# Performance work log

Measured on AMD Instinct MI355X. Metric: run time of the kernel, lower is better.

The kernel has to match this reference:

```python
import jax, jax.numpy as jnp
import numpy as np

N_TRAIN = 2000
N_ATOMS = 30
DIM_D = N_ATOMS * (N_ATOMS - 1) // 2   # 435 pairwise descriptor entries
DIM_I = 3 * N_ATOMS                    # 90 Cartesian dofs
N_PERMS = 12
SIG = 10.0

_ROWS, _COLS = np.tril_indices(N_ATOMS, -1)
_DR = np.arange(DIM_D)


def d_desc_from_comp(Rd):
    # Rd: [n, DIM_D, 3] compact pair derivatives -> full Jacobian [n, DIM_D, DIM_I]
    # each pair (a,b) contributes +d at atom a's 3 dofs and -d at atom b's.
    n = Rd.shape[0]
    out = jnp.zeros((n, DIM_D, N_ATOMS, 3), Rd.dtype)
    out = out.at[:, _DR, _ROWS, :].set(Rd)
    out = out.at[:, _DR, _COLS, :].set(-Rd)
    return out.reshape(n, DIM_D, DIM_I)


def setup_inputs() -> dict:
    key = jax.random.key(0)
    k1, k2 = jax.random.split(key)
    R_desc = jax.random.normal(k1, (N_TRAIN, DIM_D), jnp.float32)
    R_d_desc = jax.random.normal(k2, (N_TRAIN, DIM_D, 3), jnp.float32)
    # Build a permutation-consistent tril_perms_lin (identity + random atom perms).
    rng = np.random.RandomState(0)
    M = np.zeros((N_ATOMS, N_ATOMS), np.int64)
    M[_ROWS, _COLS] = np.arange(DIM_D)
    M[_COLS, _ROWS] = np.arange(DIM_D)
    tril_perms = np.empty((N_PERMS, DIM_D), np.int64)
    for p in range(N_PERMS):
        perm = np.arange(N_ATOMS) if p == 0 else rng.permutation(N_ATOMS)
        tril_perms[p] = M[perm[_ROWS], perm[_COLS]]
    tpl = (tril_perms + np.arange(N_PERMS)[:, None] * DIM_D).flatten(order='F')
    return {
        'R_desc': R_desc,
        'R_d_desc': R_d_desc,
        'tril_perms_lin': jnp.asarray(tpl),
        'j': 0,
    }


def reference(R_desc, R_d_desc, tril_perms_lin, j):
    q = np.sqrt(5.0) / SIG
    # column point j: expanded Jacobian [DIM_D, DIM_I]
    rj_d = d_desc_from_comp(R_d_desc[j][None])[0]
    # permutation-symmetrized descriptor / Jacobian for point j
    rj_desc_perms = jnp.tile(R_desc[j], N_PERMS)[tril_perms_lin].reshape(DIM_D, N_PERMS).T  # [P,D]
    rj_d_perms = jnp.tile(rj_d.T, (1, N_PERMS))[:, tril_perms_lin].reshape(DIM_I, DIM_D, N_PERMS)  # [3N,D,P]
    x_diffs = q * (R_desc[:, None, :] - rj_desc_perms[None])        # [n,P,D]
    x_dists = jnp.linalg.norm(x_diffs, axis=-1)                      # [n,P]
    exp_xs = jnp.exp(-x_dists) * (q * q / 3.0)                       # [n,P]
    exp_xs_1_x_dists = exp_xs * (1.0 + x_dists)                      # [n,P]
    # Matern-5/2 Hessian block assembly
    inner = jnp.einsum('npd,jdp->npj', x_diffs, rj_d_perms)          # [n,P,3N]
    diff_ab = jnp.einsum('npd,npj->ndj', x_diffs * exp_xs[:, :, None], inner)  # [n,D,3N]
    diff_ab = diff_ab - jnp.einsum('jdp,np->ndj', rj_d_perms, exp_xs_1_x_dists)
    Rd_full = d_desc_from_comp(R_d_desc)                             # [n,D,3N]
    k = jnp.einsum('ndj,ndk->nkj', diff_ab, Rd_full)                 # [n,3N,3N]
    return k.reshape(N_TRAIN * DIM_I, DIM_I)
```

## Files before the change

### kernel.cpp

```cpp
#include <hip/hip_runtime.h>
#include <math.h>

#define NA 30
#define ND 435
#define NI 90
#define NP 12
#define NNB (NA-1)

typedef float v2f __attribute__((ext_vector_type(2)));

struct Pre {
  int   pidx[NP][ND];
  int   pinv[NP][ND];
  int   sigma[NP][NA];
  int   sigma_inv[NP][NA];
  int   rowv[ND];
  int   colv[ND];
  int   nbr[NA][NNB];
  float rjp[NP][ND];
  float rdj[ND][3];
  unsigned int gtab[NNB][NP][NA];
  alignas(16) unsigned int stab[NA][NA][NP];
  unsigned int hmask[NA][NA];
};

__device__ __forceinline__ int pair_index(int x, int y) {
  int hi = max(x, y), lo = min(x, y);
  return hi * (hi - 1) / 2 + lo;
}

__global__ void preA_kernel(const int* __restrict__ tpl, Pre* ws) {
  const int tid = threadIdx.x;
  const int nthr = blockDim.x;

  for (int d = tid; d < ND; d += nthr) {
    int a = (int)floorf((1.0f + sqrtf(1.0f + 8.0f * (float)d)) * 0.5f);
    while (a * (a - 1) / 2 > d) --a;
    while ((a + 1) * a / 2 <= d) ++a;
    ws->rowv[d] = a;
    ws->colv[d] = d - a * (a - 1) / 2;
  }
  for (int a = tid; a < NA; a += nthr) {
    int k = 0;
    for (int u = 0; u < NA; ++u)
      if (u != a) ws->nbr[a][k++] = pair_index(a, u);
  }
  for (int idx = tid; idx < NP * ND; idx += nthr) {
    int d = idx / NP, p = idx % NP;
    ws->pidx[p][d] = tpl[idx] - p * ND;
  }
  __syncthreads();
  for (int idx = tid; idx < NP * ND; idx += nthr) {
    int d = idx / NP, p = idx % NP;
    ws->pinv[p][ws->pidx[p][d]] = d;
  }
  for (int idx = tid; idx < NP * NA; idx += nthr) {
    int p = idx / NA, a = idx % NA;
    int u1 = (a == 0) ? 1 : 0;
    int u2 = (a <= 1) ? 2 : 1;
    int e1 = ws->pidx[p][pair_index(a, u1)];
    int e2 = ws->pidx[p][pair_index(a, u2)];
    int r1 = ws->rowv[e1], c1 = ws->colv[e1];
    int r2 = ws->rowv[e2], c2 = ws->colv[e2];
    int sa = (r1 == r2 || r1 == c2) ? r1 : c1;
    ws->sigma[p][a] = sa;
  }
  __syncthreads();
  for (int idx = tid; idx < NP * NA; idx += nthr) {
    int p = idx / NA, a = idx % NA;
    ws->sigma_inv[p][ws->sigma[p][a]] = a;
  }
  __syncthreads();
  for (int it = tid; it < NA * NA; it += nthr) {
    int a = it / NA, a2 = it % NA;
    unsigned m = 0;
#pragma unroll
    for (int p = 0; p < NP; ++p)
      if (ws->sigma[p][a] == a2) m |= (1u << p);
    ws->hmask[a][a2] = m;
  }
}

__global__ void preB_kernel(const float* __restrict__ R_desc,
                            const float* __restrict__ R_d_desc,
                            const int* __restrict__ jptr,
                            Pre* ws) {
  const int gid = blockIdx.x * blockDim.x + threadIdx.x;
  const int gsz = gridDim.x * blockDim.x;
  const int j = *jptr;

  for (int idx = gid; idx < NP * ND; idx += gsz) {
    int p = idx / ND, d = idx % ND;
    ws->rjp[p][d] = R_desc[(size_t)j * ND + ws->pidx[p][d]];
  }
  for (int idx = gid; idx < ND * 3; idx += gsz)
    ((float*)ws->rdj)[idx] = R_d_desc[(size_t)j * (ND * 3) + idx];

  for (int idx = gid; idx < NNB * NP * NA; idx += gsz) {
    int a = idx % NA;
    int r = idx / NA;
    int p = r % NP, k = r / NP;
    int d  = ws->nbr[a][k];
    int di = ws->pinv[p][d];
    int d2 = ws->pidx[p][d];
    int s1 = (ws->rowv[d] == a) ? 1 : 0;
    int s2 = (ws->rowv[d2] == ws->sigma[p][a]) ? 1 : 0;
    unsigned int u = (unsigned)d | ((unsigned)di << 9) | ((unsigned)d2 << 18);
    if (s1) u |= (1u << 27);
    if (s1 == s2) u |= (1u << 28);
    ws->gtab[k][p][a] = u;
  }
  for (int idx = gid; idx < NA * NA * NP; idx += gsz) {
    int p = idx % NP;
    int r = idx / NP;
    int a2 = r % NA, a = r / NA;
    unsigned int u = 0;
    if (ws->sigma[p][a] != a2) {
      int uu = ws->sigma_inv[p][a2];
      int d1 = pair_index(a, uu);
      int d2 = ws->pidx[p][d1];
      int s1 = (ws->rowv[d1] == a) ? 1 : 0;
      int s2 = (ws->rowv[d2] == a2) ? 1 : 0;
      unsigned code = (s1 == s2) ? 1u : 2u;
      u = (unsigned)d1 | ((unsigned)d2 << 9) | (code << 18);
    }
    ws->stab[a][a2][p] = u;
  }
}

__global__ __launch_bounds__(256) void gdml_kernel(
    const float* __restrict__ R_desc,
    const float* __restrict__ R_d_desc,
    const Pre* __restrict__ ws,
    float* __restrict__ out) {
  const int n = blockIdx.x;
  const int tid = threadIdx.x;

  __shared__ float U[NP * ND];
  __shared__ float Rdn_l[ND][3];
  __shared__ float Rdj_l[ND][3];
  __shared__ float v_s[NP][NI];
  __shared__ float inner_s[NP][NI];
  __shared__ float e_s[NP], e1_s[NP];

  float* xd = U;
  float (*Hh)[NP * 9] = (float(*)[NP * 9])U;

  const float q   = 0.22360679774997896f;
  const float qq3 = 0.016666666666666666f;

  for (int idx = tid; idx < ND * 3; idx += 256) {
    ((float*)Rdn_l)[idx] = R_d_desc[(size_t)n * (ND * 3) + idx];
    ((float*)Rdj_l)[idx] = ((const float*)ws->rdj)[idx];
  }
  for (int d = tid; d < ND; d += 256) {
    float rn = R_desc[(size_t)n * ND + d];
#pragma unroll
    for (int p = 0; p < NP; ++p) xd[p * ND + d] = q * (rn - ws->rjp[p][d]);
  }
  __syncthreads();

  {
    int w = tid >> 6, lane = tid & 63;
#pragma unroll
    for (int pp = 0; pp < 3; ++pp) {
      int p = 3 * w + pp;
      float acc = 0.f;
#pragma unroll
      for (int i = 0; i < 7; ++i) {
        int d = lane + 64 * i;
        if (d < ND) { float x = xd[p * ND + d]; acc += x * x; }
      }
      for (int off = 32; off; off >>= 1) acc += __shfl_xor(acc, off);
      if (lane == 0) {
        float dist = sqrtf(acc);
        float e = expf(-dist) * qq3;
        e_s[p] = e;
        e1_s[p] = e * (1.f + dist);
      }
    }
  }
  __syncthreads();

  auto p2_item = [&](int it, float (&h)[9]) {
    int a = it % NA, p = it / NA;
    const float* xdp = xd + p * ND;
    float v0 = 0.f, v1 = 0.f, v2 = 0.f;
    float i0 = 0.f, i1 = 0.f, i2 = 0.f;
    v2f H0 = {0.f, 0.f}, H1 = {0.f, 0.f}, H2 = {0.f, 0.f};
    float Hc0 = 0.f, Hc1 = 0.f, Hc2 = 0.f;
    for (int k = 0; k < NNB; ++k) {
      unsigned int u = ws->gtab[k][p][a];
      int d  = u & 511;
      int di = (u >> 9) & 511;
      int d2 = (u >> 18) & 511;
      float s  = (u & (1u << 27)) ? 1.f : -1.f;
      float sg = (u & (1u << 28)) ? 1.f : -1.f;
      float xv = s * xdp[d];
      float xi = s * xdp[di];
      float n0 = Rdn_l[d][0], n1 = Rdn_l[d][1], n2 = Rdn_l[d][2];
      float jd0 = Rdj_l[d][0], jd1 = Rdj_l[d][1], jd2 = Rdj_l[d][2];
      float jb0 = Rdj_l[d2][0], jb1 = Rdj_l[d2][1], jb2 = Rdj_l[d2][2];
      v0 += xv * n0; v1 += xv * n1; v2 += xv * n2;
      i0 += xi * jd0; i1 += xi * jd1; i2 += xi * jd2;
      float r0 = sg * n0, r1 = sg * n1, r2 = sg * n2;
      v2f jb01 = {jb0, jb1};
      H0 += (v2f){r0, r0} * jb01; Hc0 += r0 * jb2;
      H1 += (v2f){r1, r1} * jb01; Hc1 += r1 * jb2;
      H2 += (v2f){r2, r2} * jb01; Hc2 += r2 * jb2;
    }
    float e = e_s[p];
    v_s[p][3 * a + 0] = e * v0;
    v_s[p][3 * a + 1] = e * v1;
    v_s[p][3 * a + 2] = e * v2;
    inner_s[p][3 * a + 0] = i0;
    inner_s[p][3 * a + 1] = i1;
    inner_s[p][3 * a + 2] = i2;
    h[0] = H0.x; h[1] = H0.y; h[2] = Hc0;
    h[3] = H1.x; h[4] = H1.y; h[5] = Hc1;
    h[6] = H2.x; h[7] = H2.y; h[8] = Hc2;
  };

  float h1[9], h2[9];
  const int it1 = tid;
  const int it2 = tid + 256;
  const bool has2 = (it2 < NP * NA);
  p2_item(it1, h1);
  if (has2) p2_item(it2, h2);
  __syncthreads();

  {
    int a = it1 % NA, p = it1 / NA;
    float* hb = &Hh[a][p * 9];
#pragma unroll
    for (int r = 0; r < 9; ++r) hb[r] = h1[r];
  }
  if (has2) {
    int a = it2 % NA, p = it2 / NA;
    float* hb = &Hh[a][p * 9];
#pragma unroll
    for (int r = 0; r < 9; ++r) hb[r] = h2[r];
  }
  __syncthreads();

  float e1r[NP];
#pragma unroll
  for (int p = 0; p < NP; ++p) e1r[p] = e1_s[p];

  float* outn = out + (size_t)n * (NI * NI);
  for (int it = tid; it < NA * NA; it += 256) {
    int a = it / NA, a2 = it % NA;
    v2f A0 = {0.f, 0.f}, A1 = {0.f, 0.f}, A2 = {0.f, 0.f};
    float B0 = 0.f, B1 = 0.f, B2 = 0.f;
    const uint4* st4 = (const uint4*)&ws->stab[a][a2][0];
    uint4 ua = st4[0], ub = st4[1], uc = st4[2];
    unsigned stv[12] = {ua.x, ua.y, ua.z, ua.w, ub.x, ub.y, ub.z, ub.w,
                        uc.x, uc.y, uc.z, uc.w};
#pragma unroll
    for (int p = 0; p < NP; ++p) {
      float v0 = v_s[p][3 * a + 0];
      float v1 = v_s[p][3 * a + 1];
      float v2v = v_s[p][3 * a + 2];
      float w0 = inner_s[p][3 * a2 + 0];
      float w1 = inner_s[p][3 * a2 + 1];
      float w2 = inner_s[p][3 * a2 + 2];
      v2f w01 = {w0, w1};
      A0 += (v2f){v0, v0} * w01;   B0 += v0 * w2;
      A1 += (v2f){v1, v1} * w01;   B1 += v1 * w2;
      A2 += (v2f){v2v, v2v} * w01; B2 += v2v * w2;
      unsigned u = stv[p];
      unsigned code = (u >> 18) & 3u;
      float e1 = e1r[p];
      float f = (code == 1u) ? -e1 : ((code == 2u) ? e1 : 0.f);
      int d1 = u & 511;
      int d2 = (u >> 9) & 511;
      float r0 = f * Rdn_l[d1][0];
      float r1 = f * Rdn_l[d1][1];
      float r2 = f * Rdn_l[d1][2];
      float j0 = Rdj_l[d2][0], j1 = Rdj_l[d2][1], j2 = Rdj_l[d2][2];
      v2f j01 = {j0, j1};
      A0 += (v2f){r0, r0} * j01;   B0 += r0 * j2;
      A1 += (v2f){r1, r1} * j01;   B1 += r1 * j2;
      A2 += (v2f){r2, r2} * j01;   B2 += r2 * j2;
    }
    unsigned m = ws->hmask[a][a2];
    while (m) {
      int p = __ffs(m) - 1;
      m &= m - 1;
      float e1 = e1r[p];
      const float* hb = &Hh[a][p * 9];
      A0 -= e1 * (v2f){hb[0], hb[1]}; B0 -= e1 * hb[2];
      A1 -= e1 * (v2f){hb[3], hb[4]}; B1 -= e1 * hb[5];
      A2 -= e1 * (v2f){hb[6], hb[7]}; B2 -= e1 * hb[8];
    }
    float* ob = outn + (size_t)(3 * a) * NI + 3 * a2;
    ob[0] = A0.x;          ob[1] = A0.y;          ob[2] = B0;
    ob[NI + 0] = A1.x;     ob[NI + 1] = A1.y;     ob[NI + 2] = B1;
    ob[2 * NI + 0] = A2.x; ob[2 * NI + 1] = A2.y; ob[2 * NI + 2] = B2;
  }
}

extern "C" void kernel_launch(void* const* d_in, const int* in_sizes, int n_in,
                              void* d_out, int out_size, void* d_ws, size_t ws_size,
                              hipStream_t stream) {
  const float* R_desc   = (const float*)d_in[0];
  const float* R_d_desc = (const float*)d_in[1];
  const int*   tpl      = (const int*)d_in[2];
  const int*   jptr     = (const int*)d_in[3];
  float* out = (float*)d_out;
  Pre* ws = (Pre*)d_ws;

  const int n_train = in_sizes[0] / ND;

  hipLaunchKernelGGL(preA_kernel, dim3(1), dim3(256), 0, stream, tpl, ws);
  hipLaunchKernelGGL(preB_kernel, dim3(48), dim3(256), 0, stream,
                     R_desc, R_d_desc, jptr, ws);
  hipLaunchKernelGGL(gdml_kernel, dim3(n_train), dim3(256), 0, stream,
                     R_desc, R_d_desc, ws, out);
}
```

Baseline: 110.0 us.

## Process permutations in two halves to shrink LDS and raise occupancy

The block now builds the scaled descriptor differences for six permutations at a time. This shrinks the shared x-diff buffer, and the Hessian partials reuse the same space afterward. Distance accumulation is fused into the descriptor pass using wave reductions and shared atomics, and the Jacobian and v/w arrays are padded to float4 so each read is a single vector load. Launch bounds now request 4 blocks per CU. In exchange there are more barriers, a serialized second half in which only 180 threads work, and the Hessian values are held in registers across both halves.

```diff
diff --git a/kernel.cpp b/kernel.cpp
--- a/kernel.cpp
+++ b/kernel.cpp
@@ -5,6 +5,7 @@
 #define ND 435
 #define NI 90
 #define NP 12
+#define NPH 6
 #define NNB (NA-1)
 
 typedef float v2f __attribute__((ext_vector_type(2)));
@@ -128,7 +129,7 @@
   }
 }
 
-__global__ __launch_bounds__(256) void gdml_kernel(
+__global__ __launch_bounds__(256, 4) void gdml_kernel(
     const float* __restrict__ R_desc,
     const float* __restrict__ R_d_desc,
     const Pre* __restrict__ ws,
@@ -136,110 +137,106 @@
   const int n = blockIdx.x;
   const int tid = threadIdx.x;
 
-  __shared__ float U[NP * ND];
-  __shared__ float Rdn_l[ND][3];
-  __shared__ float Rdj_l[ND][3];
-  __shared__ float v_s[NP][NI];
-  __shared__ float inner_s[NP][NI];
+  __shared__ float  U[NA * NP * 9];
+  __shared__ float4 Rdn4[ND];
+  __shared__ float4 Rdj4[ND];
+  __shared__ float4 v_s4[NP][NA];
+  __shared__ float4 w_s4[NP][NA];
+  __shared__ float dist2[NP];
   __shared__ float e_s[NP], e1_s[NP];
-
-  float* xd = U;
-  float (*Hh)[NP * 9] = (float(*)[NP * 9])U;
 
   const float q   = 0.22360679774997896f;
   const float qq3 = 0.016666666666666666f;
 
+  if (tid < NP) dist2[tid] = 0.f;
   for (int idx = tid; idx < ND * 3; idx += 256) {
-    ((float*)Rdn_l)[idx] = R_d_desc[(size_t)n * (ND * 3) + idx];
-    ((float*)Rdj_l)[idx] = ((const float*)ws->rdj)[idx];
-  }
-  for (int d = tid; d < ND; d += 256) {
-    float rn = R_desc[(size_t)n * ND + d];
-#pragma unroll
-    for (int p = 0; p < NP; ++p) xd[p * ND + d] = q * (rn - ws->rjp[p][d]);
-  }
-  __syncthreads();
-
-  {
-    int w = tid >> 6, lane = tid & 63;
-#pragma unroll
-    for (int pp = 0; pp < 3; ++pp) {
-      int p = 3 * w + pp;
-      float acc = 0.f;
-#pragma unroll
-      for (int i = 0; i < 7; ++i) {
-        int d = lane + 64 * i;
-        if (d < ND) { float x = xd[p * ND + d]; acc += x * x; }
+    int d = idx / 3, c = idx % 3;
+    ((float*)&Rdn4[d])[c] = R_d_desc[(size_t)n * (ND * 3) + idx];
+    ((float*)&Rdj4[d])[c] = ((const float*)ws->rdj)[idx];
+  }
+  __syncthreads();
+
+  float h0[9], h1[9];
+
+  auto do_half = [&](int half, float (&h)[9]) {
+    float* xd = U;
+    float acc[NPH];
+#pragma unroll
+    for (int pl = 0; pl < NPH; ++pl) acc[pl] = 0.f;
+    for (int d = tid; d < ND; d += 256) {
+      float rn = R_desc[(size_t)n * ND + d];
+#pragma unroll
+      for (int pl = 0; pl < NPH; ++pl) {
+        int p = half * NPH + pl;
+        float x = q * (rn - ws->rjp[p][d]);
+        xd[pl * ND + d] = x;
+        acc[pl] += x * x;
       }
-      for (int off = 32; off; off >>= 1) acc += __shfl_xor(acc, off);
-      if (lane == 0) {
-        float dist = sqrtf(acc);
-        float e = expf(-dist) * qq3;
-        e_s[p] = e;
-        e1_s[p] = e * (1.f + dist);
+    }
+#pragma unroll
+    for (int pl = 0; pl < NPH; ++pl) {
+      float a = acc[pl];
+      for (int off = 32; off; off >>= 1) a += __shfl_xor(a, off);
+      if ((tid & 63) == 0) atomicAdd(&dist2[half * NPH + pl], a);
+    }
+    __syncthreads();
+    if (tid < NPH) {
+      int p = half * NPH + tid;
+      float dist = sqrtf(dist2[p]);
+      float e = expf(-dist) * qq3;
+      e_s[p] = e;
+      e1_s[p] = e * (1.f + dist);
+    }
+    __syncthreads();
+
+    if (tid < NPH * NA) {
+      int a = tid % NA, pl = tid / NA;
+      int p = half * NPH + pl;
+      const float* xdp = xd + pl * ND;
+      v2f V01 = {0.f, 0.f}; float V2 = 0.f;
+      v2f I01 = {0.f, 0.f}; float I2 = 0.f;
+      v2f H0 = {0.f, 0.f}, H1 = {0.f, 0.f}, H2 = {0.f, 0.f};
+      float Hc0 = 0.f, Hc1 = 0.f, Hc2 = 0.f;
+      for (int k = 0; k < NNB; ++k) {
+        unsigned int u = ws->gtab[k][p][a];
+        int d  = u & 511;
+        int di = (u >> 9) & 511;
+        int d2 = (u >> 18) & 511;
+        float s  = (u & (1u << 27)) ? 1.f : -1.f;
+        float sg = (u & (1u << 28)) ? 1.f : -1.f;
+        float xv = s * xdp[d];
+        float xi = s * xdp[di];
+        float4 nn = Rdn4[d];
+        float4 jd = Rdj4[d];
+        float4 jb = Rdj4[d2];
+        V01 += (v2f){xv, xv} * (v2f){nn.x, nn.y}; V2 += xv * nn.z;
+        I01 += (v2f){xi, xi} * (v2f){jd.x, jd.y}; I2 += xi * jd.z;
+        float r0 = sg * nn.x, r1 = sg * nn.y, r2 = sg * nn.z;
+        v2f jb01 = {jb.x, jb.y};
+        H0 += (v2f){r0, r0} * jb01; Hc0 += r0 * jb.z;
+        H1 += (v2f){r1, r1} * jb01; Hc1 += r1 * jb.z;
+        H2 += (v2f){r2, r2} * jb01; Hc2 += r2 * jb.z;
       }
-    }
-  }
-  __syncthreads();
-
-  auto p2_item = [&](int it, float (&h)[9]) {
-    int a = it % NA, p = it / NA;
-    const float* xdp = xd + p * ND;
-    float v0 = 0.f, v1 = 0.f, v2 = 0.f;
-    float i0 = 0.f, i1 = 0.f, i2 = 0.f;
-    v2f H0 = {0.f, 0.f}, H1 = {0.f, 0.f}, H2 = {0.f, 0.f};
-    float Hc0 = 0.f, Hc1 = 0.f, Hc2 = 0.f;
-    for (int k = 0; k < NNB; ++k) {
-      unsigned int u = ws->gtab[k][p][a];
-      int d  = u & 511;
-      int di = (u >> 9) & 511;
-      int d2 = (u >> 18) & 511;
-      float s  = (u & (1u << 27)) ? 1.f : -1.f;
-      float sg = (u & (1u << 28)) ? 1.f : -1.f;
-      float xv = s * xdp[d];
-      float xi = s * xdp[di];
-      float n0 = Rdn_l[d][0], n1 = Rdn_l[d][1], n2 = Rdn_l[d][2];
-      float jd0 = Rdj_l[d][0], jd1 = Rdj_l[d][1], jd2 = Rdj_l[d][2];
-      float jb0 = Rdj_l[d2][0], jb1 = Rdj_l[d2][1], jb2 = Rdj_l[d2][2];
-      v0 += xv * n0; v1 += xv * n1; v2 += xv * n2;
-      i0 += xi * jd0; i1 += xi * jd1; i2 += xi * jd2;
-      float r0 = sg * n0, r1 = sg * n1, r2 = sg * n2;
-      v2f jb01 = {jb0, jb1};
-      H0 += (v2f){r0, r0} * jb01; Hc0 += r0 * jb2;
-      H1 += (v2f){r1, r1} * jb01; Hc1 += r1 * jb2;
-      H2 += (v2f){r2, r2} * jb01; Hc2 += r2 * jb2;
-    }
-    float e = e_s[p];
-    v_s[p][3 * a + 0] = e * v0;
-    v_s[p][3 * a + 1] = e * v1;
-    v_s[p][3 * a + 2] = e * v2;
-    inner_s[p][3 * a + 0] = i0;
-    inner_s[p][3 * a + 1] = i1;
-    inner_s[p][3 * a + 2] = i2;
-    h[0] = H0.x; h[1] = H0.y; h[2] = Hc0;
-    h[3] = H1.x; h[4] = H1.y; h[5] = Hc1;
-    h[6] = H2.x; h[7] = H2.y; h[8] = Hc2;
+      float e = e_s[p];
+      v_s4[p][a] = (float4){e * V01.x, e * V01.y, e * V2, 0.f};
+      w_s4[p][a] = (float4){I01.x, I01.y, I2, 0.f};
+      h[0] = H0.x; h[1] = H0.y; h[2] = Hc0;
+      h[3] = H1.x; h[4] = H1.y; h[5] = Hc1;
+      h[6] = H2.x; h[7] = H2.y; h[8] = Hc2;
+    }
+    __syncthreads();
   };
 
-  float h1[9], h2[9];
-  const int it1 = tid;
-  const int it2 = tid + 256;
-  const bool has2 = (it2 < NP * NA);
-  p2_item(it1, h1);
-  if (has2) p2_item(it2, h2);
-  __syncthreads();
-
-  {
-    int a = it1 % NA, p = it1 / NA;
-    float* hb = &Hh[a][p * 9];
-#pragma unroll
-    for (int r = 0; r < 9; ++r) hb[r] = h1[r];
-  }
-  if (has2) {
-    int a = it2 % NA, p = it2 / NA;
-    float* hb = &Hh[a][p * 9];
-#pragma unroll
-    for (int r = 0; r < 9; ++r) hb[r] = h2[r];
+  do_half(0, h0);
+  do_half(1, h1);
+
+  float* Hh = U;
+  if (tid < NPH * NA) {
+    int a = tid % NA, pl = tid / NA;
+#pragma unroll
+    for (int r = 0; r < 9; ++r) Hh[a * (NP * 9) + pl * 9 + r] = h0[r];
+#pragma unroll
+    for (int r = 0; r < 9; ++r) Hh[a * (NP * 9) + (NPH + pl) * 9 + r] = h1[r];
   }
   __syncthreads();
 
@@ -258,37 +255,32 @@
                         uc.x, uc.y, uc.z, uc.w};
 #pragma unroll
     for (int p = 0; p < NP; ++p) {
-      float v0 = v_s[p][3 * a + 0];
-      float v1 = v_s[p][3 * a + 1];
-      float v2v = v_s[p][3 * a + 2];
-      float w0 = inner_s[p][3 * a2 + 0];
-      float w1 = inner_s[p][3 * a2 + 1];
-      float w2 = inner_s[p][3 * a2 + 2];
-      v2f w01 = {w0, w1};
-      A0 += (v2f){v0, v0} * w01;   B0 += v0 * w2;
-      A1 += (v2f){v1, v1} * w01;   B1 += v1 * w2;
-      A2 += (v2f){v2v, v2v} * w01; B2 += v2v * w2;
+      float4 vv = v_s4[p][a];
+      float4 ww = w_s4[p][a2];
+      v2f w01 = {ww.x, ww.y};
+      A0 += (v2f){vv.x, vv.x} * w01; B0 += vv.x * ww.z;
+      A1 += (v2f){vv.y, vv.y} * w01; B1 += vv.y * ww.z;
+      A2 += (v2f){vv.z, vv.z} * w01; B2 += vv.z * ww.z;
       unsigned u = stv[p];
       unsigned code = (u >> 18) & 3u;
       float e1 = e1r[p];
       float f = (code == 1u) ? -e1 : ((code == 2u) ? e1 : 0.f);
       int d1 = u & 511;
       int d2 = (u >> 9) & 511;
-      float r0 = f * Rdn_l[d1][0];
-      float r1 = f * Rdn_l[d1][1];
-      float r2 = f * Rdn_l[d1][2];
-      float j0 = Rdj_l[d2][0], j1 = Rdj_l[d2][1], j2 = Rdj_l[d2][2];
-      v2f j01 = {j0, j1};
-      A0 += (v2f){r0, r0} * j01;   B0 += r0 * j2;
-      A1 += (v2f){r1, r1} * j01;   B1 += r1 * j2;
-      A2 += (v2f){r2, r2} * j01;   B2 += r2 * j2;
+      float4 rn1 = Rdn4[d1];
+      float4 rj2 = Rdj4[d2];
+      float r0 = f * rn1.x, r1 = f * rn1.y, r2 = f * rn1.z;
+      v2f j01 = {rj2.x, rj2.y};
+      A0 += (v2f){r0, r0} * j01; B0 += r0 * rj2.z;
+      A1 += (v2f){r1, r1} * j01; B1 += r1 * rj2.z;
+      A2 += (v2f){r2, r2} * j01; B2 += r2 * rj2.z;
     }
     unsigned m = ws->hmask[a][a2];
     while (m) {
       int p = __ffs(m) - 1;
       m &= m - 1;
       float e1 = e1r[p];
-      const float* hb = &Hh[a][p * 9];
+      const float* hb = &Hh[a * (NP * 9) + p * 9];
       A0 -= e1 * (v2f){hb[0], hb[1]}; B0 -= e1 * hb[2];
       A1 -= e1 * (v2f){hb[3], hb[4]}; B1 -= e1 * hb[5];
       A2 -= e1 * (v2f){hb[6], hb[7]}; B2 -= e1 * hb[8];
```

Result: slower. 128.7 us (+17.0%).

## Use per-atom signed Jacobian tables and sigma-indexed lookups in GDML kernel

Applied to the files above, without the earlier changes.

Replaces the compact pair-indexed Jacobian lookups and sign flags with dense per-atom signed Jacobian matrices (S for point n, Sp for point j, precomputed in workspace), so the inner loops index by neighbour atom and permuted atom instead of decoding sign bits and inverse permutations. It also fuses the squared-distance reduction into the descriptor-difference fill using per-wave partial sums and shared atomics, which removes one pass and one barrier. Launch bounds now request 3 blocks per CU. The cost is more shared memory for the expanded tables and a different store layout for w_s.

```diff
diff --git a/kernel.cpp b/kernel.cpp
--- a/kernel.cpp
+++ b/kernel.cpp
@@ -11,14 +11,12 @@
 
 struct Pre {
   int   pidx[NP][ND];
-  int   pinv[NP][ND];
   int   sigma[NP][NA];
   int   sigma_inv[NP][NA];
   int   rowv[ND];
   int   colv[ND];
-  int   nbr[NA][NNB];
   float rjp[NP][ND];
-  float rdj[ND][3];
+  alignas(16) float spj[NA][NI];
   unsigned int gtab[NNB][NP][NA];
   alignas(16) unsigned int stab[NA][NA][NP];
   unsigned int hmask[NA][NA];
@@ -40,20 +38,11 @@
     ws->rowv[d] = a;
     ws->colv[d] = d - a * (a - 1) / 2;
   }
-  for (int a = tid; a < NA; a += nthr) {
-    int k = 0;
-    for (int u = 0; u < NA; ++u)
-      if (u != a) ws->nbr[a][k++] = pair_index(a, u);
-  }
   for (int idx = tid; idx < NP * ND; idx += nthr) {
     int d = idx / NP, p = idx % NP;
     ws->pidx[p][d] = tpl[idx] - p * ND;
   }
   __syncthreads();
-  for (int idx = tid; idx < NP * ND; idx += nthr) {
-    int d = idx / NP, p = idx % NP;
-    ws->pinv[p][ws->pidx[p][d]] = d;
-  }
   for (int idx = tid; idx < NP * NA; idx += nthr) {
     int p = idx / NA, a = idx % NA;
     int u1 = (a == 0) ? 1 : 0;
@@ -93,42 +82,40 @@
     int p = idx / ND, d = idx % ND;
     ws->rjp[p][d] = R_desc[(size_t)j * ND + ws->pidx[p][d]];
   }
-  for (int idx = gid; idx < ND * 3; idx += gsz)
-    ((float*)ws->rdj)[idx] = R_d_desc[(size_t)j * (ND * 3) + idx];
-
+  for (int idx = gid; idx < NA * NI; idx += gsz) {
+    int a = idx / NI, r = idx % NI;
+    int u = r / 3, c = r % 3;
+    float val = 0.f;
+    if (u != a) {
+      int d = pair_index(a, u);
+      float t = R_d_desc[(size_t)j * (ND * 3) + 3 * d + c];
+      val = (a > u) ? t : -t;
+    }
+    ((float*)ws->spj)[idx] = val;
+  }
   for (int idx = gid; idx < NNB * NP * NA; idx += gsz) {
     int a = idx % NA;
     int r = idx / NA;
     int p = r % NP, k = r / NP;
-    int d  = ws->nbr[a][k];
-    int di = ws->pinv[p][d];
-    int d2 = ws->pidx[p][d];
-    int s1 = (ws->rowv[d] == a) ? 1 : 0;
-    int s2 = (ws->rowv[d2] == ws->sigma[p][a]) ? 1 : 0;
-    unsigned int u = (unsigned)d | ((unsigned)di << 9) | ((unsigned)d2 << 18);
-    if (s1) u |= (1u << 27);
-    if (s1 == s2) u |= (1u << 28);
-    ws->gtab[k][p][a] = u;
+    int u = k + (k >= a ? 1 : 0);
+    int d = pair_index(a, u);
+    int su = ws->sigma[p][u];
+    ws->gtab[k][p][a] = (unsigned)d | ((unsigned)u << 9) | ((unsigned)su << 14);
   }
   for (int idx = gid; idx < NA * NA * NP; idx += gsz) {
     int p = idx % NP;
     int r = idx / NP;
     int a2 = r % NA, a = r / NA;
-    unsigned int u = 0;
+    unsigned int v = 0;
     if (ws->sigma[p][a] != a2) {
-      int uu = ws->sigma_inv[p][a2];
-      int d1 = pair_index(a, uu);
-      int d2 = ws->pidx[p][d1];
-      int s1 = (ws->rowv[d1] == a) ? 1 : 0;
-      int s2 = (ws->rowv[d2] == a2) ? 1 : 0;
-      unsigned code = (s1 == s2) ? 1u : 2u;
-      u = (unsigned)d1 | ((unsigned)d2 << 9) | (code << 18);
-    }
-    ws->stab[a][a2][p] = u;
-  }
-}
-
-__global__ __launch_bounds__(256) void gdml_kernel(
+      int u = ws->sigma_inv[p][a2];
+      v = (unsigned)u | ((unsigned)ws->sigma[p][a] << 5) | (1u << 31);
+    }
+    ws->stab[a][a2][p] = v;
+  }
+}
+
+__global__ __launch_bounds__(256, 3) void gdml_kernel(
     const float* __restrict__ R_desc,
     const float* __restrict__ R_d_desc,
     const Pre* __restrict__ ws,
@@ -137,85 +124,94 @@
   const int tid = threadIdx.x;
 
   __shared__ float U[NP * ND];
-  __shared__ float Rdn_l[ND][3];
-  __shared__ float Rdj_l[ND][3];
-  __shared__ float v_s[NP][NI];
-  __shared__ float inner_s[NP][NI];
+  __shared__ float S[NA * NI];
+  __shared__ alignas(16) float Sp[NA * NI];
+  __shared__ float v_s[NP * NI];
+  __shared__ float w_s[NP * NI];
+  __shared__ float dist2[NP];
   __shared__ float e_s[NP], e1_s[NP];
-
-  float* xd = U;
-  float (*Hh)[NP * 9] = (float(*)[NP * 9])U;
 
   const float q   = 0.22360679774997896f;
   const float qq3 = 0.016666666666666666f;
 
-  for (int idx = tid; idx < ND * 3; idx += 256) {
-    ((float*)Rdn_l)[idx] = R_d_desc[(size_t)n * (ND * 3) + idx];
-    ((float*)Rdj_l)[idx] = ((const float*)ws->rdj)[idx];
-  }
-  for (int d = tid; d < ND; d += 256) {
-    float rn = R_desc[(size_t)n * ND + d];
-#pragma unroll
-    for (int p = 0; p < NP; ++p) xd[p * ND + d] = q * (rn - ws->rjp[p][d]);
-  }
-  __syncthreads();
-
+  if (tid < NP) dist2[tid] = 0.f;
   {
-    int w = tid >> 6, lane = tid & 63;
-#pragma unroll
-    for (int pp = 0; pp < 3; ++pp) {
-      int p = 3 * w + pp;
-      float acc = 0.f;
-#pragma unroll
-      for (int i = 0; i < 7; ++i) {
-        int d = lane + 64 * i;
-        if (d < ND) { float x = xd[p * ND + d]; acc += x * x; }
+    const float4* g4 = (const float4*)ws->spj;
+    float4* s4 = (float4*)Sp;
+    for (int idx = tid; idx < (NA * NI) / 4; idx += 256) s4[idx] = g4[idx];
+  }
+  for (int idx = tid; idx < NA * NI; idx += 256) {
+    int a = idx / NI, r = idx % NI;
+    int u = r / 3, c = r % 3;
+    float val = 0.f;
+    if (u != a) {
+      int d = pair_index(a, u);
+      float t = R_d_desc[(size_t)n * (ND * 3) + 3 * d + c];
+      val = (a > u) ? t : -t;
+    }
+    S[idx] = val;
+  }
+  {
+    float acc[NP];
+#pragma unroll
+    for (int p = 0; p < NP; ++p) acc[p] = 0.f;
+    for (int d = tid; d < ND; d += 256) {
+      float rn = R_desc[(size_t)n * ND + d];
+#pragma unroll
+      for (int p = 0; p < NP; ++p) {
+        float x = q * (rn - ws->rjp[p][d]);
+        U[p * ND + d] = x;
+        acc[p] += x * x;
       }
-      for (int off = 32; off; off >>= 1) acc += __shfl_xor(acc, off);
-      if (lane == 0) {
-        float dist = sqrtf(acc);
-        float e = expf(-dist) * qq3;
-        e_s[p] = e;
-        e1_s[p] = e * (1.f + dist);
-      }
-    }
+    }
+#pragma unroll
+    for (int p = 0; p < NP; ++p) {
+      float a = acc[p];
+      for (int off = 32; off; off >>= 1) a += __shfl_xor(a, off);
+      if ((tid & 63) == 0) atomicAdd(&dist2[p], a);
+    }
+  }
+  __syncthreads();
+  if (tid < NP) {
+    float dist = sqrtf(dist2[tid]);
+    float e = expf(-dist) * qq3;
+    e_s[tid] = e;
+    e1_s[tid] = e * (1.f + dist);
   }
   __syncthreads();
 
   auto p2_item = [&](int it, float (&h)[9]) {
     int a = it % NA, p = it / NA;
-    const float* xdp = xd + p * ND;
-    float v0 = 0.f, v1 = 0.f, v2 = 0.f;
-    float i0 = 0.f, i1 = 0.f, i2 = 0.f;
+    int sa = ws->sigma[p][a];
+    const float* xdp = U + p * ND;
+    const float* Srow = S + a * NI;
+    const float* Prow = Sp + sa * NI;
+    v2f V01 = {0.f, 0.f}; float V2 = 0.f;
+    v2f I01 = {0.f, 0.f}; float I2 = 0.f;
     v2f H0 = {0.f, 0.f}, H1 = {0.f, 0.f}, H2 = {0.f, 0.f};
     float Hc0 = 0.f, Hc1 = 0.f, Hc2 = 0.f;
     for (int k = 0; k < NNB; ++k) {
-      unsigned int u = ws->gtab[k][p][a];
-      int d  = u & 511;
-      int di = (u >> 9) & 511;
-      int d2 = (u >> 18) & 511;
-      float s  = (u & (1u << 27)) ? 1.f : -1.f;
-      float sg = (u & (1u << 28)) ? 1.f : -1.f;
-      float xv = s * xdp[d];
-      float xi = s * xdp[di];
-      float n0 = Rdn_l[d][0], n1 = Rdn_l[d][1], n2 = Rdn_l[d][2];
-      float jd0 = Rdj_l[d][0], jd1 = Rdj_l[d][1], jd2 = Rdj_l[d][2];
-      float jb0 = Rdj_l[d2][0], jb1 = Rdj_l[d2][1], jb2 = Rdj_l[d2][2];
-      v0 += xv * n0; v1 += xv * n1; v2 += xv * n2;
-      i0 += xi * jd0; i1 += xi * jd1; i2 += xi * jd2;
-      float r0 = sg * n0, r1 = sg * n1, r2 = sg * n2;
-      v2f jb01 = {jb0, jb1};
-      H0 += (v2f){r0, r0} * jb01; Hc0 += r0 * jb2;
-      H1 += (v2f){r1, r1} * jb01; Hc1 += r1 * jb2;
-      H2 += (v2f){r2, r2} * jb01; Hc2 += r2 * jb2;
+      unsigned g = ws->gtab[k][p][a];
+      int d  = g & 511;
+      int u  = (g >> 9) & 31;
+      int su = (g >> 14) & 31;
+      float x  = xdp[d];
+      float s0 = Srow[3 * u], s1 = Srow[3 * u + 1], s2 = Srow[3 * u + 2];
+      float t0 = Prow[3 * su], t1 = Prow[3 * su + 1], t2 = Prow[3 * su + 2];
+      V01 += (v2f){x, x} * (v2f){s0, s1}; V2 += x * s2;
+      I01 += (v2f){x, x} * (v2f){t0, t1}; I2 += x * t2;
+      v2f t01 = {t0, t1};
+      H0 += (v2f){s0, s0} * t01; Hc0 += s0 * t2;
+      H1 += (v2f){s1, s1} * t01; Hc1 += s1 * t2;
+      H2 += (v2f){s2, s2} * t01; Hc2 += s2 * t2;
     }
     float e = e_s[p];
-    v_s[p][3 * a + 0] = e * v0;
-    v_s[p][3 * a + 1] = e * v1;
-    v_s[p][3 * a + 2] = e * v2;
-    inner_s[p][3 * a + 0] = i0;
-    inner_s[p][3 * a + 1] = i1;
-    inner_s[p][3 * a + 2] = i2;
+    v_s[p * NI + 3 * a + 0] = e * V01.x;
+    v_s[p * NI + 3 * a + 1] = e * V01.y;
+    v_s[p * NI + 3 * a + 2] = e * V2;
+    w_s[p * NI + 3 * sa + 0] = I01.x;
+    w_s[p * NI + 3 * sa + 1] = I01.y;
+    w_s[p * NI + 3 * sa + 2] = I2;
     h[0] = H0.x; h[1] = H0.y; h[2] = Hc0;
     h[3] = H1.x; h[4] = H1.y; h[5] = Hc1;
     h[6] = H2.x; h[7] = H2.y; h[8] = Hc2;
@@ -231,13 +227,13 @@
 
   {
     int a = it1 % NA, p = it1 / NA;
-    float* hb = &Hh[a][p * 9];
+    float* hb = U + a * (NP * 9) + p * 9;
 #pragma unroll
     for (int r = 0; r < 9; ++r) hb[r] = h1[r];
   }
   if (has2) {
     int a = it2 % NA, p = it2 / NA;
-    float* hb = &Hh[a][p * 9];
+    float* hb = U + a * (NP * 9) + p * 9;
 #pragma unroll
     for (int r = 0; r < 9; ++r) hb[r] = h2[r];
   }
@@ -252,43 +248,44 @@
     int a = it / NA, a2 = it % NA;
     v2f A0 = {0.f, 0.f}, A1 = {0.f, 0.f}, A2 = {0.f, 0.f};
     float B0 = 0.f, B1 = 0.f, B2 = 0.f;
+    const float* Srow = S + a * NI;
     const uint4* st4 = (const uint4*)&ws->stab[a][a2][0];
     uint4 ua = st4[0], ub = st4[1], uc = st4[2];
     unsigned stv[12] = {ua.x, ua.y, ua.z, ua.w, ub.x, ub.y, ub.z, ub.w,
                         uc.x, uc.y, uc.z, uc.w};
 #pragma unroll
     for (int p = 0; p < NP; ++p) {
-      float v0 = v_s[p][3 * a + 0];
-      float v1 = v_s[p][3 * a + 1];
-      float v2v = v_s[p][3 * a + 2];
-      float w0 = inner_s[p][3 * a2 + 0];
-      float w1 = inner_s[p][3 * a2 + 1];
-      float w2 = inner_s[p][3 * a2 + 2];
+      float v0 = v_s[p * NI + 3 * a + 0];
+      float v1 = v_s[p * NI + 3 * a + 1];
+      float v2v = v_s[p * NI + 3 * a + 2];
+      float w0 = w_s[p * NI + 3 * a2 + 0];
+      float w1 = w_s[p * NI + 3 * a2 + 1];
+      float w2 = w_s[p * NI + 3 * a2 + 2];
       v2f w01 = {w0, w1};
       A0 += (v2f){v0, v0} * w01;   B0 += v0 * w2;
       A1 += (v2f){v1, v1} * w01;   B1 += v1 * w2;
       A2 += (v2f){v2v, v2v} * w01; B2 += v2v * w2;
-      unsigned u = stv[p];
-      unsigned code = (u >> 18) & 3u;
-      float e1 = e1r[p];
-      float f = (code == 1u) ? -e1 : ((code == 2u) ? e1 : 0.f);
-      int d1 = u & 511;
-      int d2 = (u >> 9) & 511;
-      float r0 = f * Rdn_l[d1][0];
-      float r1 = f * Rdn_l[d1][1];
-      float r2 = f * Rdn_l[d1][2];
-      float j0 = Rdj_l[d2][0], j1 = Rdj_l[d2][1], j2 = Rdj_l[d2][2];
+      unsigned g = stv[p];
+      float f = (g >> 31) ? e1r[p] : 0.f;
+      int u  = g & 31;
+      int sa = (g >> 5) & 31;
+      float r0 = f * Srow[3 * u];
+      float r1 = f * Srow[3 * u + 1];
+      float r2 = f * Srow[3 * u + 2];
+      float j0 = Sp[sa * NI + 3 * a2 + 0];
+      float j1 = Sp[sa * NI + 3 * a2 + 1];
+      float j2 = Sp[sa * NI + 3 * a2 + 2];
       v2f j01 = {j0, j1};
-      A0 += (v2f){r0, r0} * j01;   B0 += r0 * j2;
-      A1 += (v2f){r1, r1} * j01;   B1 += r1 * j2;
-      A2 += (v2f){r2, r2} * j01;   B2 += r2 * j2;
+      A0 += (v2f){r0, r0} * j01; B0 += r0 * j2;
+      A1 += (v2f){r1, r1} * j01; B1 += r1 * j2;
+      A2 += (v2f){r2, r2} * j01; B2 += r2 * j2;
     }
     unsigned m = ws->hmask[a][a2];
     while (m) {
       int p = __ffs(m) - 1;
       m &= m - 1;
       float e1 = e1r[p];
-      const float* hb = &Hh[a][p * 9];
+      const float* hb = U + a * (NP * 9) + p * 9;
       A0 -= e1 * (v2f){hb[0], hb[1]}; B0 -= e1 * hb[2];
       A1 -= e1 * (v2f){hb[3], hb[4]}; B1 -= e1 * hb[5];
       A2 -= e1 * (v2f){hb[6], hb[7]}; B2 -= e1 * hb[8];
```

Result: slower. 155.8 us (+41.6%).
